# Kernel optimization log

Measured on AMD Instinct MI355X. Metric: run time of the kernel, lower is better.

Reference implementation:

```python
import jax, jax.numpy as jnp
import numpy as np
import math

B, S, D, H = 256, 200, 256, 8
DH = D // H
EPS = 1e-6
GELU_C = math.sqrt(2.0 / math.pi)


def layer_norm(x, a, b):
    # torch LayerNorm variant: unbiased std, eps added to std (not var)
    mean = jnp.mean(x, axis=-1, keepdims=True)
    std = jnp.sqrt(jnp.var(x, axis=-1, keepdims=True, ddof=1))
    return a * (x - mean) / (std + EPS) + b


def setup_inputs() -> dict:
    key = jax.random.key(0)
    ks = jax.random.split(key, 12)
    s = 0.02
    return {
        "hidden_img": jax.random.normal(ks[0], (B, S, D), jnp.float32),
        "hidden_title": jax.random.normal(ks[1], (B, S, D), jnp.float32),
        "mask": jax.random.randint(ks[2], (B, S), 0, 2, jnp.int32),
        "a_img": jnp.ones((D,), jnp.float32),
        "b_img": jnp.zeros((D,), jnp.float32),
        "a_title": jnp.ones((D,), jnp.float32),
        "b_title": jnp.zeros((D,), jnp.float32),
        "Wb": jax.random.normal(ks[3], (D, D), jnp.float32) * s,
        "bb": jnp.zeros((D,), jnp.float32),
        "Wo": jax.random.normal(ks[4], (D, D), jnp.float32) * s,
        "bo": jnp.zeros((D,), jnp.float32),
        "scale_attn": jax.random.normal(ks[5], (H, S), jnp.float32) * 0.5 + 1.0,
        "a_out": jnp.ones((D,), jnp.float32),
        "b_out": jnp.zeros((D,), jnp.float32),
        "W1": jax.random.normal(ks[6], (D, D), jnp.float32) * s,
        "b1": jnp.zeros((D,), jnp.float32),
        "scale_ffn": jax.random.normal(ks[7], (S, 1), jnp.float32) * 0.5 + 1.0,
    }


def reference(hidden_img, hidden_title, mask, a_img, b_img, a_title, b_title,
              Wb, bb, Wo, bo, scale_attn, a_out, b_out, W1, b1, scale_ffn):
    img_n = layer_norm(hidden_img, a_img, b_img)      # q = k = v
    title_n = layer_norm(hidden_title, a_title, b_title)

    # heads
    qkv = img_n.reshape(B, S, H, DH)                   # bshd
    k_b = (title_n @ Wb.T + bb).reshape(B, S, H, DH)

    # scores: q.k + q.k_b, scaled, per-head/per-query learned scale
    corr = jnp.einsum("bqhd,bkhd->bhqk", qkv, qkv)
    corr = corr + jnp.einsum("bqhd,bkhd->bhqk", qkv, k_b)
    corr = corr / math.sqrt(DH)
    corr = corr * scale_attn[None, :, :, None]         # [1,H,S,1]

    # key mask [B,S] -> [B,1,1,S]
    corr = jnp.where(mask[:, None, None, :] == 0, -1e9, corr)
    prob = jax.nn.softmax(corr, axis=-1)

    ctx = jnp.einsum("bhqk,bkhd->bqhd", prob, qkv).reshape(B, S, D)
    attn_out = ctx @ Wo.T + bo

    # residual 1 (dropout is identity in eval)
    h1 = hidden_img + attn_out

    # pre-norm FFN with learned positional scale + tanh-GELU
    h1_n = layer_norm(h1, a_out, b_out)
    z = scale_ffn[None] * (h1_n @ W1.T + b1)           # [B,S,D]
    act = 0.5 * z * (1.0 + jnp.tanh(GELU_C * (z + 0.044715 * z ** 3)))

    return h1 + act
```

## Files before the change

### kernel.cpp

```cpp
#include <hip/hip_runtime.h>
#include <math.h>

#define B_ 256
#define S_ 200
#define D_ 256
#define H_ 8
#define DH_ 32
#define BS_ (B_*S_)
#define NEL ((size_t)BS_*D_)

typedef __attribute__((ext_vector_type(8))) short bhalf8;
typedef __attribute__((ext_vector_type(4))) float fx4;

__device__ __forceinline__ unsigned short f2bf(float f) {
  union { float f; unsigned u; } x; x.f = f;
  unsigned r = x.u + 0x7FFFu + ((x.u >> 16) & 1u);
  return (unsigned short)(r >> 16);
}
__device__ __forceinline__ float bf2f(unsigned short h) {
  union { unsigned u; float f; } x; x.u = ((unsigned)h) << 16; return x.f;
}
__device__ __forceinline__ bhalf8 pack8(float4 a, float4 b) {
  bhalf8 p;
  p[0] = (short)f2bf(a.x); p[1] = (short)f2bf(a.y);
  p[2] = (short)f2bf(a.z); p[3] = (short)f2bf(a.w);
  p[4] = (short)f2bf(b.x); p[5] = (short)f2bf(b.y);
  p[6] = (short)f2bf(b.z); p[7] = (short)f2bf(b.w);
  return p;
}
__device__ __forceinline__ float wave_reduce_sum(float v) {
#pragma unroll
  for (int o = 32; o >= 1; o >>= 1) v += __shfl_xor(v, o, 64);
  return v;
}

__global__ __launch_bounds__(256) void conv_w_kernel(
    const float* __restrict__ Wb, const float* __restrict__ Wo,
    const float* __restrict__ W1, short* __restrict__ dst) {
  const int t = blockIdx.x * 256 + threadIdx.x;
  const int w = t >> 13, r = (t & 8191) * 8;
  const float* src = (w == 0) ? Wb : ((w == 1) ? Wo : W1);
  float4 f0 = *(const float4*)(src + r), f1 = *(const float4*)(src + r + 4);
  *(bhalf8*)(dst + (w << 16) + r) = pack8(f0, f1);
}

__global__ __launch_bounds__(256) void ln2_kernel(
    const float* __restrict__ ximg, const float* __restrict__ xtit,
    const float* __restrict__ a_img, const float* __restrict__ b_img,
    const float* __restrict__ a_tit, const float* __restrict__ b_tit,
    short* __restrict__ yimg, short* __restrict__ ytit) {
  const int wave = threadIdx.x >> 6, lane = threadIdx.x & 63;
  const int second = (blockIdx.x >= BS_ / 4) ? 1 : 0;
  const int row = (blockIdx.x - second * (BS_ / 4)) * 4 + wave;
  const float* x = second ? xtit : ximg;
  const float* a = second ? a_tit : a_img;
  const float* b = second ? b_tit : b_img;
  short* y = second ? ytit : yimg;
  float4 v = ((const float4*)(x + (size_t)row * D_))[lane];
  float s  = v.x + v.y + v.z + v.w;
  float ss = v.x*v.x + v.y*v.y + v.z*v.z + v.w*v.w;
  s = wave_reduce_sum(s); ss = wave_reduce_sum(ss);
  float mean = s * (1.0f / D_);
  float var  = fmaxf((ss - (float)D_ * mean * mean) * (1.0f / (D_ - 1)), 0.0f);
  float inv  = 1.0f / (sqrtf(var) + 1e-6f);
  float4 av = ((const float4*)a)[lane];
  float4 bv = ((const float4*)b)[lane];
  ushort4 o;
  o.x = f2bf(av.x * (v.x - mean) * inv + bv.x);
  o.y = f2bf(av.y * (v.y - mean) * inv + bv.y);
  o.z = f2bf(av.z * (v.z - mean) * inv + bv.z);
  o.w = f2bf(av.w * (v.w - mean) * inv + bv.w);
  *(ushort4*)(y + (size_t)row * D_ + lane * 4) = o;
}

template <int EPI>
__global__ __launch_bounds__(512, 2) void gemm_k(
    const short* __restrict__ A, const short* __restrict__ W,
    const float* __restrict__ bias,
    const short* __restrict__ addb,
    const float* __restrict__ addf,
    const float* __restrict__ ga, const float* __restrict__ gb,
    const float* __restrict__ sf,
    short* __restrict__ outb, float* __restrict__ outf) {
  __shared__ short Ws[256 * 260];
  const int tid = threadIdx.x;
  for (int cid = tid; cid < 8192; cid += 512) {
    const int row = cid >> 5, ch = cid & 31;
    *(bhalf8*)&Ws[row * 260 + ch * 8] = *(const bhalf8*)(W + row * 256 + ch * 8);
  }
  __syncthreads();

  const int wv = tid >> 6, lane = tid & 63, g = lane >> 4, cc = lane & 15;
  const int mrow0 = blockIdx.x * 256 + wv * 32;
  fx4 acc[2][16];
#pragma unroll
  for (int i = 0; i < 2; i++)
#pragma unroll
    for (int j = 0; j < 16; j++) acc[i][j] = (fx4){0.f, 0.f, 0.f, 0.f};

  bhalf8 a0 = *(const bhalf8*)(A + (size_t)(mrow0 + cc) * D_ + g * 8);
  bhalf8 a1 = *(const bhalf8*)(A + (size_t)(mrow0 + 16 + cc) * D_ + g * 8);
#pragma unroll
  for (int kc = 0; kc < 8; kc++) {
    bhalf8 n0, n1;
    if (kc < 7) {
      n0 = *(const bhalf8*)(A + (size_t)(mrow0 + cc) * D_ + (kc + 1) * 32 + g * 8);
      n1 = *(const bhalf8*)(A + (size_t)(mrow0 + 16 + cc) * D_ + (kc + 1) * 32 + g * 8);
    }
#pragma unroll
    for (int j = 0; j < 16; j++) {
      bhalf8 fb = *(const bhalf8*)&Ws[(j * 16 + cc) * 260 + kc * 32 + g * 8];
      acc[0][j] = __builtin_amdgcn_mfma_f32_16x16x32_bf16(a0, fb, acc[0][j], 0, 0, 0);
      acc[1][j] = __builtin_amdgcn_mfma_f32_16x16x32_bf16(a1, fb, acc[1][j], 0, 0, 0);
    }
    a0 = n0; a1 = n1;
  }

  float bias_r[16];
#pragma unroll
  for (int j = 0; j < 16; j++) bias_r[j] = bias[j * 16 + cc];

  if (EPI == 0) {
#pragma unroll
    for (int i = 0; i < 2; i++)
#pragma unroll
      for (int r = 0; r < 4; r++) {
        const size_t m = mrow0 + i * 16 + 4 * g + r;
#pragma unroll
        for (int j = 0; j < 16; j++) {
          const int n = j * 16 + cc;
          float v = acc[i][j][r] + bias_r[j] + bf2f((unsigned short)addb[m * D_ + n]);
          outb[m * D_ + n] = (short)f2bf(v);
        }
      }
  } else if (EPI == 1) {
    float ga_r[16], gb_r[16];
#pragma unroll
    for (int j = 0; j < 16; j++) { ga_r[j] = ga[j * 16 + cc]; gb_r[j] = gb[j * 16 + cc]; }
#pragma unroll
    for (int i = 0; i < 2; i++)
#pragma unroll
      for (int r = 0; r < 4; r++) {
        const size_t m = mrow0 + i * 16 + 4 * g + r;
        float s = 0.f, ss = 0.f;
#pragma unroll
        for (int j = 0; j < 16; j++) {
          const int n = j * 16 + cc;
          float v = acc[i][j][r] + bias_r[j] + addf[m * D_ + n];
          outf[m * D_ + n] = v;
          acc[i][j][r] = v;
          s += v; ss += v * v;
        }
        s  += __shfl_xor(s, 1);  s += __shfl_xor(s, 2);  s += __shfl_xor(s, 4);  s += __shfl_xor(s, 8);
        ss += __shfl_xor(ss, 1); ss += __shfl_xor(ss, 2); ss += __shfl_xor(ss, 4); ss += __shfl_xor(ss, 8);
        const float mean = s * (1.0f / D_);
        const float var  = fmaxf((ss * (1.0f / D_) - mean * mean) * ((float)D_ / (D_ - 1)), 0.0f);
        const float inv  = 1.0f / (sqrtf(var) + 1e-6f);
#pragma unroll
        for (int j = 0; j < 16; j++) {
          const int n = j * 16 + cc;
          float h = (acc[i][j][r] - mean) * inv * ga_r[j] + gb_r[j];
          outb[m * D_ + n] = (short)f2bf(h);
        }
      }
  } else {
#pragma unroll
    for (int i = 0; i < 2; i++)
#pragma unroll
      for (int r = 0; r < 4; r++) {
        const size_t m = mrow0 + i * 16 + 4 * g + r;
        const float sfr = sf[(int)(m % S_)];
#pragma unroll
        for (int j = 0; j < 16; j++) {
          const int n = j * 16 + cc;
          float z = (acc[i][j][r] + bias_r[j]) * sfr;
          float gl = 0.5f * z * (1.0f + tanhf(0.79788456080286536f * (z + 0.044715f * z * z * z)));
          outf[m * D_ + n] = addf[m * D_ + n] + gl;
        }
      }
  }
}

__global__ __launch_bounds__(256) void attn_mfma_kernel(
    const short* __restrict__ imgb, const short* __restrict__ kkb,
    const int* __restrict__ mask, const float* __restrict__ scale_attn,
    short* __restrict__ ctxb) {
  __shared__ short K_s[208 * 40];
  __shared__ short Vt_s[32 * 232];
  __shared__ short P_s[4][16 * 232];
  __shared__ int   m_s[224];
  const int tid = threadIdx.x;
  const int b = blockIdx.x >> 3, h = blockIdx.x & 7;
  const size_t base2 = (size_t)(b * S_) * D_ + h * DH_;

  for (int i = tid; i < 800; i += 256) {
    const int row = i >> 2, ch = i & 3;
    *(bhalf8*)&K_s[row * 40 + ch * 8] = *(const bhalf8*)(kkb + base2 + (size_t)row * D_ + ch * 8);
  }
  for (int t = tid; t < 400; t += 256) {
    const int p = t >> 2, ch = t & 3;
    bhalf8 lo = *(const bhalf8*)(imgb + base2 + (size_t)(2 * p) * D_ + ch * 8);
    bhalf8 hi = *(const bhalf8*)(imgb + base2 + (size_t)(2 * p + 1) * D_ + ch * 8);
#pragma unroll
    for (int u = 0; u < 8; u++) {
      unsigned dw = (unsigned)(unsigned short)lo[u] | ((unsigned)(unsigned short)hi[u] << 16);
      *(unsigned*)&Vt_s[(ch * 8 + u) * 232 + 2 * p] = dw;
    }
  }
  { const int row = 200 + (tid >> 5), col = tid & 31; K_s[row * 40 + col] = 0; }
  { const int row = tid >> 3, k0 = 200 + (tid & 7) * 4;
    *(unsigned long long*)&Vt_s[row * 232 + k0] = 0ULL; }
  if (tid < 224) m_s[tid] = (tid < S_) ? mask[b * S_ + tid] : 0;

  const int wv = tid >> 6, lane = tid & 63;
  const int g = lane >> 4, c = lane & 15;
  short* Pw = &P_s[wv][0];
  { const int row = lane >> 2, colq = lane & 3;
    *(unsigned long long*)&Pw[row * 232 + 208 + colq * 4] = 0ULL; }
  __syncthreads();

  const float rs32 = 0.17677669529663687f;
  const fx4 zero = {0.f, 0.f, 0.f, 0.f};
  for (int t = wv; t < 13; t += 4) {
    const int q0 = t * 16;
    int qr = q0 + c; if (qr > S_ - 1) qr = S_ - 1;
    bhalf8 af = *(const bhalf8*)(imgb + base2 + (size_t)qr * D_ + g * 8);

    fx4 st[13];
    __builtin_amdgcn_s_setprio(1);
#pragma unroll
    for (int t2 = 0; t2 < 13; t2++) {
      bhalf8 kf = *(const bhalf8*)&K_s[(t2 * 16 + c) * 40 + g * 8];
      st[t2] = __builtin_amdgcn_mfma_f32_16x16x32_bf16(af, kf, zero, 0, 0, 0);
    }
    __builtin_amdgcn_s_setprio(0);
    float sc[4], mx[4], l[4];
#pragma unroll
    for (int r = 0; r < 4; r++) {
      int q = q0 + 4 * g + r; if (q > S_ - 1) q = S_ - 1;
      sc[r] = scale_attn[h * S_ + q] * rs32;
      mx[r] = -1e30f; l[r] = 0.f;
    }
#pragma unroll
    for (int t2 = 0; t2 < 13; t2++) {
      const int msk = m_s[t2 * 16 + c];
#pragma unroll
      for (int r = 0; r < 4; r++) {
        float s = (msk != 0) ? st[t2][r] * sc[r] : -1e30f;
        st[t2][r] = s;
        mx[r] = fmaxf(mx[r], s);
      }
    }
#pragma unroll
    for (int r = 0; r < 4; r++) {
      mx[r] = fmaxf(mx[r], __shfl_xor(mx[r], 1));
      mx[r] = fmaxf(mx[r], __shfl_xor(mx[r], 2));
      mx[r] = fmaxf(mx[r], __shfl_xor(mx[r], 4));
      mx[r] = fmaxf(mx[r], __shfl_xor(mx[r], 8));
    }
#pragma unroll
    for (int t2 = 0; t2 < 13; t2++) {
#pragma unroll
      for (int r = 0; r < 4; r++) {
        float p = __expf(st[t2][r] - mx[r]);
        l[r] += p;
        Pw[(4 * g + r) * 232 + t2 * 16 + c] = (short)f2bf(p);
      }
    }
#pragma unroll
    for (int r = 0; r < 4; r++) {
      l[r] += __shfl_xor(l[r], 1);
      l[r] += __shfl_xor(l[r], 2);
      l[r] += __shfl_xor(l[r], 4);
      l[r] += __shfl_xor(l[r], 8);
    }
    fx4 o0 = zero, o1 = zero;
    __builtin_amdgcn_s_setprio(1);
#pragma unroll
    for (int ch = 0; ch < 7; ch++) {
      bhalf8 pf = *(const bhalf8*)&Pw[c * 232 + ch * 32 + g * 8];
      bhalf8 v0 = *(const bhalf8*)&Vt_s[c * 232 + ch * 32 + g * 8];
      bhalf8 v1 = *(const bhalf8*)&Vt_s[(16 + c) * 232 + ch * 32 + g * 8];
      o0 = __builtin_amdgcn_mfma_f32_16x16x32_bf16(pf, v0, o0, 0, 0, 0);
      o1 = __builtin_amdgcn_mfma_f32_16x16x32_bf16(pf, v1, o1, 0, 0, 0);
    }
    __builtin_amdgcn_s_setprio(0);
#pragma unroll
    for (int r = 0; r < 4; r++) {
      const int q = q0 + 4 * g + r;
      if (q < S_) {
        const float inv = 1.0f / l[r];
        ctxb[base2 + (size_t)q * D_ + c]      = (short)f2bf(o0[r] * inv);
        ctxb[base2 + (size_t)q * D_ + 16 + c] = (short)f2bf(o1[r] * inv);
      }
    }
  }
}

extern "C" void kernel_launch(void* const* d_in, const int* in_sizes, int n_in,
                              void* d_out, int out_size, void* d_ws, size_t ws_size,
                              hipStream_t stream) {
  const float* hidden_img   = (const float*)d_in[0];
  const float* hidden_title = (const float*)d_in[1];
  const int*   mask         = (const int*)d_in[2];
  const float* a_img   = (const float*)d_in[3];
  const float* b_img   = (const float*)d_in[4];
  const float* a_title = (const float*)d_in[5];
  const float* b_title = (const float*)d_in[6];
  const float* Wb = (const float*)d_in[7];
  const float* bb = (const float*)d_in[8];
  const float* Wo = (const float*)d_in[9];
  const float* bo = (const float*)d_in[10];
  const float* scale_attn = (const float*)d_in[11];
  const float* a_out = (const float*)d_in[12];
  const float* b_out = (const float*)d_in[13];
  const float* W1 = (const float*)d_in[14];
  const float* b1 = (const float*)d_in[15];
  const float* scale_ffn = (const float*)d_in[16];
  float* out = (float*)d_out;

  char* wsb = (char*)d_ws;
  short* img_nb = (short*)(wsb);
  short* kkb    = (short*)(wsb + 26214400);
  short* ctxb   = (short*)(wsb + 52428800);
  float* h1     = (float*)(wsb + 78643200);
  short* h1nb   = (short*)(wsb + 131072000);
  short* w16    = (short*)(wsb + 157286400);

  conv_w_kernel<<<dim3(96), 256, 0, stream>>>(Wb, Wo, W1, w16);
  ln2_kernel<<<dim3(2 * BS_ / 4), 256, 0, stream>>>(hidden_img, hidden_title,
      a_img, b_img, a_title, b_title, img_nb, ctxb);
  gemm_k<0><<<dim3(200), 512, 0, stream>>>(ctxb, w16, bb, img_nb,
      nullptr, nullptr, nullptr, nullptr, kkb, nullptr);
  attn_mfma_kernel<<<dim3(B_ * H_), 256, 0, stream>>>(img_nb, kkb, mask, scale_attn, ctxb);
  gemm_k<1><<<dim3(200), 512, 0, stream>>>(ctxb, w16 + 65536, bo, nullptr,
      hidden_img, a_out, b_out, nullptr, h1nb, h1);
  gemm_k<2><<<dim3(200), 512, 0, stream>>>(h1nb, w16 + 131072, b1, nullptr,
      h1, nullptr, nullptr, scale_ffn, nullptr, out);
}
```

Measured before the change: 397.7 us.

## Drop LDS weight staging in GEMMs and store residual h1 as bf16

The GEMM kernel stops staging the full 256x256 bf16 weight matrix in shared memory. It preloads all A fragments into registers and streams weight fragments straight from global/L2, using 256-thread blocks and twice as many blocks. The intermediate residual h1 is now written and read as bf16 instead of fp32, roughly halving that tensor's traffic. The cost is lower precision in the residual added to the output and more register pressure and L2 weight reads per wave.

```diff
diff --git a/kernel.cpp b/kernel.cpp
--- a/kernel.cpp
+++ b/kernel.cpp
@@ -74,46 +74,39 @@
 }
 
 template <int EPI>
-__global__ __launch_bounds__(512, 2) void gemm_k(
+__global__ __launch_bounds__(256, 2) void gemm_k(
     const short* __restrict__ A, const short* __restrict__ W,
     const float* __restrict__ bias,
     const short* __restrict__ addb,
     const float* __restrict__ addf,
     const float* __restrict__ ga, const float* __restrict__ gb,
     const float* __restrict__ sf,
-    short* __restrict__ outb, float* __restrict__ outf) {
-  __shared__ short Ws[256 * 260];
+    short* __restrict__ outb, short* __restrict__ outb2,
+    float* __restrict__ outf) {
   const int tid = threadIdx.x;
-  for (int cid = tid; cid < 8192; cid += 512) {
-    const int row = cid >> 5, ch = cid & 31;
-    *(bhalf8*)&Ws[row * 260 + ch * 8] = *(const bhalf8*)(W + row * 256 + ch * 8);
-  }
-  __syncthreads();
-
   const int wv = tid >> 6, lane = tid & 63, g = lane >> 4, cc = lane & 15;
-  const int mrow0 = blockIdx.x * 256 + wv * 32;
+  const int mrow0 = blockIdx.x * 128 + wv * 32;
+
+  bhalf8 a[2][8];
+#pragma unroll
+  for (int kc = 0; kc < 8; kc++) {
+    a[0][kc] = *(const bhalf8*)(A + (size_t)(mrow0 + cc) * D_ + kc * 32 + g * 8);
+    a[1][kc] = *(const bhalf8*)(A + (size_t)(mrow0 + 16 + cc) * D_ + kc * 32 + g * 8);
+  }
   fx4 acc[2][16];
 #pragma unroll
   for (int i = 0; i < 2; i++)
 #pragma unroll
     for (int j = 0; j < 16; j++) acc[i][j] = (fx4){0.f, 0.f, 0.f, 0.f};
 
-  bhalf8 a0 = *(const bhalf8*)(A + (size_t)(mrow0 + cc) * D_ + g * 8);
-  bhalf8 a1 = *(const bhalf8*)(A + (size_t)(mrow0 + 16 + cc) * D_ + g * 8);
-#pragma unroll
-  for (int kc = 0; kc < 8; kc++) {
-    bhalf8 n0, n1;
-    if (kc < 7) {
-      n0 = *(const bhalf8*)(A + (size_t)(mrow0 + cc) * D_ + (kc + 1) * 32 + g * 8);
-      n1 = *(const bhalf8*)(A + (size_t)(mrow0 + 16 + cc) * D_ + (kc + 1) * 32 + g * 8);
-    }
-#pragma unroll
-    for (int j = 0; j < 16; j++) {
-      bhalf8 fb = *(const bhalf8*)&Ws[(j * 16 + cc) * 260 + kc * 32 + g * 8];
-      acc[0][j] = __builtin_amdgcn_mfma_f32_16x16x32_bf16(a0, fb, acc[0][j], 0, 0, 0);
-      acc[1][j] = __builtin_amdgcn_mfma_f32_16x16x32_bf16(a1, fb, acc[1][j], 0, 0, 0);
-    }
-    a0 = n0; a1 = n1;
+#pragma unroll
+  for (int j = 0; j < 16; j++) {
+#pragma unroll
+    for (int kc = 0; kc < 8; kc++) {
+      bhalf8 fb = *(const bhalf8*)(W + (size_t)(j * 16 + cc) * D_ + kc * 32 + g * 8);
+      acc[0][j] = __builtin_amdgcn_mfma_f32_16x16x32_bf16(a[0][kc], fb, acc[0][j], 0, 0, 0);
+      acc[1][j] = __builtin_amdgcn_mfma_f32_16x16x32_bf16(a[1][kc], fb, acc[1][j], 0, 0, 0);
+    }
   }
 
   float bias_r[16];
@@ -145,9 +138,8 @@
         float s = 0.f, ss = 0.f;
 #pragma unroll
         for (int j = 0; j < 16; j++) {
-          const int n = j * 16 + cc;
-          float v = acc[i][j][r] + bias_r[j] + addf[m * D_ + n];
-          outf[m * D_ + n] = v;
+          float v = acc[i][j][r] + bias_r[j] + addf[m * D_ + j * 16 + cc];
+          outb2[m * D_ + j * 16 + cc] = (short)f2bf(v);
           acc[i][j][r] = v;
           s += v; ss += v * v;
         }
@@ -158,9 +150,8 @@
         const float inv  = 1.0f / (sqrtf(var) + 1e-6f);
 #pragma unroll
         for (int j = 0; j < 16; j++) {
-          const int n = j * 16 + cc;
           float h = (acc[i][j][r] - mean) * inv * ga_r[j] + gb_r[j];
-          outb[m * D_ + n] = (short)f2bf(h);
+          outb[m * D_ + j * 16 + cc] = (short)f2bf(h);
         }
       }
   } else {
@@ -175,7 +166,7 @@
           const int n = j * 16 + cc;
           float z = (acc[i][j][r] + bias_r[j]) * sfr;
           float gl = 0.5f * z * (1.0f + tanhf(0.79788456080286536f * (z + 0.044715f * z * z * z)));
-          outf[m * D_ + n] = addf[m * D_ + n] + gl;
+          outf[m * D_ + n] = bf2f((unsigned short)addb[m * D_ + n]) + gl;
         }
       }
   }
@@ -323,18 +314,18 @@
   short* img_nb = (short*)(wsb);
   short* kkb    = (short*)(wsb + 26214400);
   short* ctxb   = (short*)(wsb + 52428800);
-  float* h1     = (float*)(wsb + 78643200);
-  short* h1nb   = (short*)(wsb + 131072000);
-  short* w16    = (short*)(wsb + 157286400);
+  short* h1b    = (short*)(wsb + 78643200);
+  short* h1nb   = (short*)(wsb + 104857600);
+  short* w16    = (short*)(wsb + 131072000);
 
   conv_w_kernel<<<dim3(96), 256, 0, stream>>>(Wb, Wo, W1, w16);
   ln2_kernel<<<dim3(2 * BS_ / 4), 256, 0, stream>>>(hidden_img, hidden_title,
       a_img, b_img, a_title, b_title, img_nb, ctxb);
-  gemm_k<0><<<dim3(200), 512, 0, stream>>>(ctxb, w16, bb, img_nb,
-      nullptr, nullptr, nullptr, nullptr, kkb, nullptr);
+  gemm_k<0><<<dim3(400), 256, 0, stream>>>(ctxb, w16, bb, img_nb,
+      nullptr, nullptr, nullptr, nullptr, kkb, nullptr, nullptr);
   attn_mfma_kernel<<<dim3(B_ * H_), 256, 0, stream>>>(img_nb, kkb, mask, scale_attn, ctxb);
-  gemm_k<1><<<dim3(200), 512, 0, stream>>>(ctxb, w16 + 65536, bo, nullptr,
-      hidden_img, a_out, b_out, nullptr, h1nb, h1);
-  gemm_k<2><<<dim3(200), 512, 0, stream>>>(h1nb, w16 + 131072, b1, nullptr,
-      h1, nullptr, nullptr, scale_ffn, nullptr, out);
-}
+  gemm_k<1><<<dim3(400), 256, 0, stream>>>(ctxb, w16 + 65536, bo, nullptr,
+      hidden_img, a_out, b_out, nullptr, h1nb, h1b, nullptr);
+  gemm_k<2><<<dim3(400), 256, 0, stream>>>(h1nb, w16 + 131072, b1, h1b,
+      nullptr, nullptr, nullptr, scale_ffn, nullptr, nullptr, out);
+}
```

Measured after the change: 425.9 us. 7.1% more time.
